# Optimization experiments

Hardware: AMD Instinct MI355X
Metric: run time of the kernel (lower is better)

Reference implementation:

```python
import jax, jax.numpy as jnp
import numpy as np

B, S, HID = 2, 2048, 2048
H, HK, D = 16, 4, 128  # num_heads, num_kv_heads, head_dim
G = H // HK            # GQA group size


def _make_rope(B, S, D):
    pos = jnp.arange(S, dtype=jnp.float32)
    inv_freq = 1.0 / (10000.0 ** (jnp.arange(0, D, 2, dtype=jnp.float32) / D))
    freqs = pos[:, None] * inv_freq[None, :]          # [S, D/2]
    emb = jnp.concatenate([freqs, freqs], axis=-1)     # [S, D]
    cos = jnp.broadcast_to(jnp.cos(emb)[None], (B, S, D))
    sin = jnp.broadcast_to(jnp.sin(emb)[None], (B, S, D))
    return cos, sin


def setup_inputs() -> dict:
    key = jax.random.key(0)
    k0, k1, k2 = jax.random.split(key, 3)
    hidden_states = jax.random.normal(k0, (B, S, HID), dtype=jnp.float32)
    cos, sin = _make_rope(B, S, D)
    w_qkv = jax.random.normal(k1, ((H + 2 * HK) * D, HID), dtype=jnp.float32) * 0.02
    b_qkv = jnp.zeros(((H + 2 * HK) * D,), dtype=jnp.float32)
    w_o = jax.random.normal(k2, (HID, HID), dtype=jnp.float32) * 0.02
    b_o = jnp.zeros((HID,), dtype=jnp.float32)
    return {"hidden_states": hidden_states, "cos": cos, "sin": sin,
            "w_qkv": w_qkv, "b_qkv": b_qkv, "w_o": w_o, "b_o": b_o}


def _rotate_half(x):
    x1, x2 = jnp.split(x, 2, axis=-1)
    return jnp.concatenate([-x2, x1], axis=-1)


def reference(hidden_states, cos, sin, w_qkv, b_qkv, w_o, b_o):
    b, s, _ = hidden_states.shape
    qkv = jnp.einsum('bsh,oh->bso', hidden_states, w_qkv) + b_qkv
    q, k, v = jnp.split(qkv, [H * D, (H + HK) * D], axis=-1)
    # [B, heads, S, D]
    q = q.reshape(b, s, H, D).transpose(0, 2, 1, 3)
    k = k.reshape(b, s, HK, D).transpose(0, 2, 1, 3)
    v = v.reshape(b, s, HK, D).transpose(0, 2, 1, 3)
    # RoPE (cos/sin broadcast over head axis)
    c = cos[:, None, :, :]
    sn = sin[:, None, :, :]
    q = q * c + _rotate_half(q) * sn
    k = k * c + _rotate_half(k) * sn
    # GQA attention without materializing repeated K/V: group q heads
    qg = q.reshape(b, HK, G, s, D)
    scale = 1.0 / jnp.sqrt(jnp.float32(D))
    scores = jnp.einsum('bkgqd,bkpd->bkgqp', qg, k) * scale  # [B,HK,G,S,S]
    probs = jax.nn.softmax(scores, axis=-1)
    out = jnp.einsum('bkgqp,bkpd->bkgqd', probs, v)           # [B,HK,G,S,D]
    out = out.reshape(b, H, s, D).transpose(0, 2, 1, 3).reshape(b, s, H * D)
    return jnp.einsum('bsh,oh->bso', out, w_o) + b_o
```

## Files before the change

kernel.cpp:

```cpp
#include <hip/hip_runtime.h>
#include <hip/hip_bf16.h>
#include <stdint.h>

typedef __bf16 bf16x8 __attribute__((ext_vector_type(8)));
typedef float f32x4 __attribute__((ext_vector_type(4)));
typedef float f32x16 __attribute__((ext_vector_type(16)));
typedef float f32x4v __attribute__((ext_vector_type(4)));
typedef unsigned short u16;
typedef unsigned int u32;
typedef u16 u16x8 __attribute__((ext_vector_type(8)));
typedef u32 u32x4 __attribute__((ext_vector_type(4)));

#define B_ 2
#define S_ 2048
#define HID_ 2048
#define H_ 16
#define HK_ 4
#define D_ 128
#define NQKV_ 3072

__device__ __forceinline__ u16 f2bf(float f) {
  u32 u = __builtin_bit_cast(u32, f);
  u32 r = (u + 0x7fffu + ((u >> 16) & 1u)) >> 16;
  return (u16)r;
}
__device__ __forceinline__ float bf2f(u16 v) {
  u32 u = ((u32)v) << 16;
  return __builtin_bit_cast(float, u);
}
__device__ __forceinline__ u32 cvtpk(float lo, float hi) {
  u32 r;
  asm("v_cvt_pk_bf16_f32 %0, %1, %2" : "=v"(r) : "v"(lo), "v"(hi));
  return r;
}
__device__ __forceinline__ void gload_lds16(const void* g, void* l) {
  __builtin_amdgcn_global_load_lds((const __attribute__((address_space(1))) void*)g,
                                   (__attribute__((address_space(3))) void*)l, 16, 0, 0);
}

__global__ __launch_bounds__(256) void k_cvt3(const float* __restrict__ a, u16* __restrict__ oa, int na,
                                              const float* __restrict__ b, u16* __restrict__ ob, int nb,
                                              const float* __restrict__ c, u16* __restrict__ oc, int nc) {
  int total = na + nb + nc;
  for (int i = blockIdx.x * 256 + threadIdx.x; i < total; i += gridDim.x * 256) {
    const float* src;
    u16* dst;
    int j = i;
    if (j < na) { src = a; dst = oa; }
    else if (j < na + nb) { j -= na; src = b; dst = ob; }
    else { j -= na + nb; src = c; dst = oc; }
    const f32x4v* p = (const f32x4v*)(src + (size_t)j * 8);
    f32x4v x = p[0], y = p[1];
    u16x8 w;
    w[0] = f2bf(x[0]); w[1] = f2bf(x[1]); w[2] = f2bf(x[2]); w[3] = f2bf(x[3]);
    w[4] = f2bf(y[0]); w[5] = f2bf(y[1]); w[6] = f2bf(y[2]); w[7] = f2bf(y[3]);
    *(u16x8*)(dst + (size_t)j * 8) = w;
  }
}

template <int ISSUES>
__device__ __forceinline__ void stage_half(const u16* __restrict__ src, int K, char* ldsb, int tid) {
#pragma unroll
  for (int i = 0; i < ISSUES; ++i) {
    int off = i * 8192 + tid * 16;
    int r = off >> 7, cb = off & 127;
    int scb = cb ^ ((r & 7) << 4);
    gload_lds16((const char*)(src + (size_t)r * K) + scb, ldsb + i * 8192 + (tid & ~63) * 16);
  }
}

template <int BM, typename CT>
__global__ __launch_bounds__(512, 1) void k_gemm8p(const u16* __restrict__ A, const u16* __restrict__ Bm,
                                                   const float* __restrict__ bias, CT* __restrict__ C,
                                                   int M, int N, int K) {
  constexpr int HAR = BM / 2;
  constexpr int AHB = HAR * 128;
  constexpr int AISS = AHB / 8192;
  constexpr int MREP = BM / 32;
  constexpr int MQ = MREP / 4;
  constexpr int DB = 2 * AHB + 32768;
  __shared__ __attribute__((aligned(16))) char lds[2 * DB];
  const int tid = threadIdx.x, lane = tid & 63;
  const int wid = tid >> 6, wm = wid >> 2, wn = wid & 3;
  const int l15 = lane & 15, l4 = lane >> 4;
  const int nwg = gridDim.x * gridDim.y;
  const int bid = blockIdx.y * gridDim.x + blockIdx.x;
  const int wgid = (bid & 7) * (nwg >> 3) + (bid >> 3);
  const int bx = wgid % gridDim.x, by = wgid / gridDim.x;
  const int row0 = by * BM, col0 = bx * 256;
  const int NT = K >> 6;

  f32x4 acc[MREP][4] = {};

  auto stageA = [&](int t, int h) {
    stage_half<AISS>(A + (size_t)(row0 + h * HAR) * K + t * 64, K, lds + (t & 1) * DB + h * AHB, tid);
  };
  auto stageB = [&](int t, int h) {
    stage_half<2>(Bm + (size_t)(col0 + h * 128) * K + t * 64, K, lds + (t & 1) * DB + 2 * AHB + h * 16384, tid);
  };

  stageA(0, 0); stageA(0, 1); stageB(0, 0); stageB(0, 1);
  if (NT > 1) { stageB(1, 0); stageB(1, 1); }
  if (NT > 1) asm volatile("s_waitcnt vmcnt(4)" ::: "memory");
  else        asm volatile("s_waitcnt vmcnt(0)" ::: "memory");
  __builtin_amdgcn_s_barrier();

  const char* myA = lds + wm * AHB;
  const char* myB = lds + 2 * AHB + (wn >> 1) * 16384;
  const int rBb = (wn & 1) * 64;

  for (int t = 0; t < NT; ++t) {
    const int d = t & 1;
    const char* Ab = myA + d * DB;
    const char* Bb = myB + d * DB;
    bf16x8 bfr[4][2];
#pragma unroll
    for (int j = 0; j < 4; ++j) {
      if (j == 0) {
#pragma unroll
        for (int n = 0; n < 4; ++n)
#pragma unroll
          for (int ks = 0; ks < 2; ++ks) {
            int r = rBb + n * 16 + l15;
            bfr[n][ks] = *(const bf16x8*)(Bb + r * 128 + ((ks * 64 + l4 * 16) ^ ((r & 7) << 4)));
          }
      }
      bf16x8 afr[MQ][2];
#pragma unroll
      for (int mq = 0; mq < MQ; ++mq)
#pragma unroll
        for (int ks = 0; ks < 2; ++ks) {
          int r = (j * MQ + mq) * 16 + l15;
          afr[mq][ks] = *(const bf16x8*)(Ab + r * 128 + ((ks * 64 + l4 * 16) ^ ((r & 7) << 4)));
        }
      if (j == 0) { if (t + 1 < NT) stageA(t + 1, 0); }
      else if (j == 1) { if (t + 1 < NT) stageA(t + 1, 1); }
      else if (j == 2) { if (t + 2 < NT) stageB(t + 2, 0); }
      else {
        if (t + 2 < NT) { stageB(t + 2, 1); asm volatile("s_waitcnt vmcnt(4)" ::: "memory"); }
        else             asm volatile("s_waitcnt vmcnt(0)" ::: "memory");
      }
      __builtin_amdgcn_s_barrier();
      asm volatile("s_waitcnt lgkmcnt(0)" ::: "memory");
      __builtin_amdgcn_s_setprio(1);
#pragma unroll
      for (int mq = 0; mq < MQ; ++mq)
#pragma unroll
        for (int ks = 0; ks < 2; ++ks)
#pragma unroll
          for (int n = 0; n < 4; ++n)
            acc[j * MQ + mq][n] =
                __builtin_amdgcn_mfma_f32_16x16x32_bf16(afr[mq][ks], bfr[n][ks], acc[j * MQ + mq][n], 0, 0, 0);
      __builtin_amdgcn_s_setprio(0);
      __builtin_amdgcn_s_barrier();
    }
  }

#pragma unroll
  for (int m = 0; m < MREP; ++m) {
    int grow = row0 + wm * HAR + m * 16 + l4 * 4;
#pragma unroll
    for (int n = 0; n < 4; ++n) {
      int gcol = col0 + wn * 64 + n * 16 + l15;
      float bv = bias[gcol];
#pragma unroll
      for (int r2 = 0; r2 < 4; ++r2) {
        float v = acc[m][n][r2] + bv;
        if constexpr (sizeof(CT) == 2) C[(size_t)(grow + r2) * N + gcol] = (CT)f2bf(v);
        else                           C[(size_t)(grow + r2) * N + gcol] = v;
      }
    }
  }
}

__global__ __launch_bounds__(256) void k_rope_split(const u16* __restrict__ qkv,
                                                    const float* __restrict__ cosb,
                                                    const float* __restrict__ sinb,
                                                    u16* __restrict__ Qb, u16* __restrict__ Kb,
                                                    u16* __restrict__ Vt) {
  const int bs = blockIdx.x;
  const int b = bs >> 11, s = bs & 2047;
  const size_t base = (size_t)bs * NQKV_;
  const size_t cs = (size_t)bs * D_;
  const int tid = threadIdx.x;
  const float qscale = 0.08838834764831845f;

  if (tid < 160) {
    const bool isq = tid < 128;
    const int idx = isq ? tid : (tid - 128);
    const int hh = idx >> 3, d0 = (idx & 7) * 8;
    const size_t srcb = base + (isq ? 0 : H_ * D_) + hh * D_;
    bf16x8 x1 = *(const bf16x8*)(qkv + srcb + d0);
    bf16x8 x2 = *(const bf16x8*)(qkv + srcb + d0 + 64);
    u16x8 y1, y2;
    const u16x8 u1 = __builtin_bit_cast(u16x8, x1);
    const u16x8 u2 = __builtin_bit_cast(u16x8, x2);
    const float sc = isq ? qscale : 1.0f;
#pragma unroll
    for (int i = 0; i < 8; ++i) {
      float f1 = bf2f(u1[i]), f2 = bf2f(u2[i]);
      float c1 = cosb[cs + d0 + i], s1 = sinb[cs + d0 + i];
      float c2 = cosb[cs + 64 + d0 + i], s2 = sinb[cs + 64 + d0 + i];
      y1[i] = f2bf((f1 * c1 - f2 * s1) * sc);
      y2[i] = f2bf((f2 * c2 + f1 * s2) * sc);
    }
    size_t o;
    if (isq) o = ((size_t)(b * H_ + hh) * S_ + s) * D_ + d0;
    else     o = ((size_t)(b * HK_ + hh) * S_ + s) * D_ + d0;
    u16* dst = isq ? Qb : Kb;
    *(u16x8*)(dst + o) = y1;
    *(u16x8*)(dst + o + 64) = y2;
  } else if (tid < 224) {
    const int idx = tid - 160;
    const int hk = idx >> 4, d0 = (idx & 15) * 8;
    bf16x8 xv = *(const bf16x8*)(qkv + base + (H_ + HK_) * D_ + hk * D_ + d0);
    const u16x8 uv = __builtin_bit_cast(u16x8, xv);
    u16* vb = Vt + (size_t)(b * HK_ + hk) * D_ * S_ + s;
#pragma unroll
    for (int i = 0; i < 8; ++i) vb[(size_t)(d0 + i) * S_] = uv[i];
  }
}

__global__ __launch_bounds__(512, 2) void k_attn(const u16* __restrict__ Qb, const u16* __restrict__ Kb,
                                                 const u16* __restrict__ Vt, u16* __restrict__ Ob) {
  __shared__ __attribute__((aligned(16))) char lds[65536];
  const int qt = blockIdx.x;
  const int bh = blockIdx.y;
  const int b = bh >> 4, h = bh & 15, hk = h >> 2;
  const int tid = threadIdx.x, lane = tid & 63, wid = tid >> 6;
  const int l31 = lane & 31, hi = lane >> 5;
  const int g = wid >> 2, wq = wid & 3;

  const int qrow = qt * 128 + wq * 32 + l31;
  const u16* qptr = Qb + ((size_t)(b * H_ + h) * S_ + qrow) * D_;
  bf16x8 qf[8];
#pragma unroll
  for (int ks = 0; ks < 8; ++ks) qf[ks] = *(const bf16x8*)(qptr + ks * 16 + hi * 8);

  const u16* kbase = Kb + (size_t)(b * HK_ + hk) * S_ * D_;
  const u16* vbase = Vt + (size_t)(b * HK_ + hk) * D_ * S_;
  char* gbase = lds + g * 32768;

  int krow[4], kc[4], vrow[4], vc[4];
#pragma unroll
  for (int i = 0; i < 4; ++i) {
    int s = (tid & 255) + i * 256;
    krow[i] = s >> 4; kc[i] = s & 15;
    vrow[i] = s >> 3; vc[i] = s & 7;
  }

  f32x16 o[4] = {};
  float mrun = -1e30f, lrun = 0.f;

  bf16x8 kreg[4], vreg[4];
  auto load_tile = [&](int tt) {
#pragma unroll
    for (int i = 0; i < 4; ++i) {
      kreg[i] = *(const bf16x8*)(kbase + (size_t)(tt * 64 + krow[i]) * D_ + kc[i] * 8);
      vreg[i] = *(const bf16x8*)(vbase + (size_t)vrow[i] * S_ + tt * 64 + vc[i] * 8);
    }
  };
  auto write_tile = [&]() {
#pragma unroll
    for (int i = 0; i < 4; ++i) {
      *(bf16x8*)(gbase + ((krow[i] * 256 + kc[i] * 16) ^ ((krow[i] & 15) << 4))) = kreg[i];
      *(bf16x8*)(gbase + 16384 + ((vrow[i] * 128 + vc[i] * 16) ^ ((vrow[i] & 7) << 4))) = vreg[i];
    }
  };

  const int t0 = g * 16;
  load_tile(t0);
  write_tile();
  __syncthreads();

  for (int t = 0; t < 16; ++t) {
    if (t < 15) load_tile(t0 + t + 1);

    f32x16 sc[2] = {};
    __builtin_amdgcn_s_setprio(1);
#pragma unroll
    for (int ks = 0; ks < 8; ++ks) {
#pragma unroll
      for (int T = 0; T < 2; ++T) {
        int row = T * 32 + l31;
        bf16x8 kf = *(const bf16x8*)(gbase + ((row * 256 + ks * 32 + hi * 16) ^ ((row & 15) << 4)));
        sc[T] = __builtin_amdgcn_mfma_f32_32x32x16_bf16(kf, qf[ks], sc[T], 0, 0, 0);
      }
    }
    __builtin_amdgcn_s_setprio(0);

    float pmax = sc[0][0];
#pragma unroll
    for (int r = 1; r < 16; ++r) pmax = fmaxf(pmax, sc[0][r]);
#pragma unroll
    for (int r = 0; r < 16; ++r) pmax = fmaxf(pmax, sc[1][r]);
    pmax = fmaxf(pmax, __shfl_xor(pmax, 32));
    if (__any(pmax > mrun + 8.f)) {
      float mn = fmaxf(mrun, pmax);
      float alpha = __expf(mrun - mn);
      mrun = mn;
      lrun *= alpha;
#pragma unroll
      for (int dt = 0; dt < 4; ++dt)
#pragma unroll
        for (int r = 0; r < 16; ++r) o[dt][r] *= alpha;
    }
    float rs = 0.f;
#pragma unroll
    for (int T = 0; T < 2; ++T)
#pragma unroll
      for (int r = 0; r < 16; ++r) {
        float p = __expf(sc[T][r] - mrun);
        sc[T][r] = p;
        rs += p;
      }
    rs += __shfl_xor(rs, 32);
    lrun += rs;

    bf16x8 pf[4];
#pragma unroll
    for (int T = 0; T < 2; ++T) {
#pragma unroll
      for (int gg = 0; gg < 2; ++gg) {
        u32 a0 = cvtpk(sc[T][8 * gg + 0], sc[T][8 * gg + 1]);
        u32 a1 = cvtpk(sc[T][8 * gg + 2], sc[T][8 * gg + 3]);
        u32 a2 = cvtpk(sc[T][8 * gg + 4], sc[T][8 * gg + 5]);
        u32 a3 = cvtpk(sc[T][8 * gg + 6], sc[T][8 * gg + 7]);
        u32 x0 = (u32)__shfl_xor((int)a0, 32);
        u32 x1 = (u32)__shfl_xor((int)a1, 32);
        u32 x2 = (u32)__shfl_xor((int)a2, 32);
        u32 x3 = (u32)__shfl_xor((int)a3, 32);
        u32 s0 = hi ? x2 : a0;
        u32 s1 = hi ? x3 : a1;
        u32 s2 = hi ? a2 : x0;
        u32 s3 = hi ? a3 : x1;
        u32x4 w = {s0, s1, s2, s3};
        pf[T * 2 + gg] = __builtin_bit_cast(bf16x8, w);
      }
    }

    __builtin_amdgcn_s_setprio(1);
#pragma unroll
    for (int ks2 = 0; ks2 < 4; ++ks2) {
#pragma unroll
      for (int dt = 0; dt < 4; ++dt) {
        int row = dt * 32 + l31;
        bf16x8 vf = *(const bf16x8*)(gbase + 16384 + ((row * 128 + ks2 * 32 + hi * 16) ^ ((row & 7) << 4)));
        o[dt] = __builtin_amdgcn_mfma_f32_32x32x16_bf16(vf, pf[ks2], o[dt], 0, 0, 0);
      }
    }
    __builtin_amdgcn_s_setprio(0);

    __syncthreads();
    if (t < 15) write_tile();
    __syncthreads();
  }

  float2* mlb = (float2*)(lds + 32768);
  if (g == 1) {
    char* myp = lds + wq * 8192;
#pragma unroll
    for (int dt = 0; dt < 4; ++dt)
#pragma unroll
      for (int t = 0; t < 8; ++t)
        *(u32*)(myp + (dt * 8 + t) * 256 + lane * 4) = cvtpk(o[dt][2 * t], o[dt][2 * t + 1]);
    if (!hi) mlb[wq * 32 + l31] = float2{mrun, lrun};
  }
  __syncthreads();
  float inv = 0.f;
  if (g == 0) {
    float2 ml1 = mlb[wq * 32 + l31];
    float m = fmaxf(mrun, ml1.x);
    float a0 = __expf(mrun - m), a1 = __expf(ml1.x - m);
    float lt = lrun * a0 + ml1.y * a1;
    inv = 1.0f / lt;
    char* myp = lds + wq * 8192;
#pragma unroll
    for (int dt = 0; dt < 4; ++dt)
#pragma unroll
      for (int t = 0; t < 8; ++t) {
        u32 w = *(const u32*)(myp + (dt * 8 + t) * 256 + lane * 4);
        float plo = bf2f((u16)(w & 0xffffu));
        float phi = bf2f((u16)(w >> 16));
        o[dt][2 * t]     = o[dt][2 * t] * a0 + plo * a1;
        o[dt][2 * t + 1] = o[dt][2 * t + 1] * a0 + phi * a1;
      }
  }
  __syncthreads();

  if (g == 0) {
    char* myreg = lds + wq * 8192;
#pragma unroll
    for (int dt = 0; dt < 4; ++dt)
#pragma unroll
      for (int t = 0; t < 8; ++t) {
        u32 w = cvtpk(o[dt][2 * t] * inv, o[dt][2 * t + 1] * inv);
        int d0 = dt * 32 + 2 * (t & 1) + 8 * (t >> 1) + 4 * hi;
        *(u32*)(myreg + ((l31 * 256 + d0 * 2) ^ ((l31 & 15) << 4))) = w;
      }
    asm volatile("s_waitcnt lgkmcnt(0)");
    {
      int q = lane >> 1, hf = lane & 1;
      int srow = qt * 128 + wq * 32 + q;
      u16* orow = Ob + ((size_t)(b * S_ + srow)) * HID_ + h * 128 + hf * 64;
#pragma unroll
      for (int i = 0; i < 8; ++i) {
        bf16x8 vv = *(const bf16x8*)(myreg + ((q * 256 + hf * 128 + i * 16) ^ ((q & 15) << 4)));
        *(bf16x8*)(orow + i * 8) = vv;
      }
    }
  }
}

extern "C" void kernel_launch(void* const* d_in, const int* in_sizes, int n_in,
                              void* d_out, int out_size, void* d_ws, size_t ws_size,
                              hipStream_t stream) {
  const float* hs = (const float*)d_in[0];
  const float* cosb = (const float*)d_in[1];
  const float* sinb = (const float*)d_in[2];
  const float* w_qkv = (const float*)d_in[3];
  const float* b_qkv = (const float*)d_in[4];
  const float* w_o = (const float*)d_in[5];
  const float* b_o = (const float*)d_in[6];
  float* out = (float*)d_out;

  char* ws = (char*)d_ws;
  u16* Xb    = (u16*)ws;
  u16* Wqkvb = (u16*)(ws + 16777216);
  u16* Wob   = (u16*)(ws + 29360128);
  u16* qkvb  = (u16*)(ws + 37748736);
  u16* Qb    = (u16*)(ws + 62914560);
  u16* Kb    = (u16*)(ws + 79691776);
  u16* Vt    = (u16*)(ws + 83886080);
  u16* Ob = Xb;

  hipLaunchKernelGGL(k_cvt3, dim3(2048), dim3(256), 0, stream,
                     hs, Xb, (B_ * S_ * HID_) / 8,
                     w_qkv, Wqkvb, (NQKV_ * HID_) / 8,
                     w_o, Wob, (HID_ * HID_) / 8);
  hipLaunchKernelGGL((k_gemm8p<256, u16>), dim3(NQKV_ / 256, (B_ * S_) / 256), dim3(512), 0, stream,
                     Xb, Wqkvb, b_qkv, qkvb, B_ * S_, NQKV_, HID_);
  hipLaunchKernelGGL(k_rope_split, dim3(B_ * S_), dim3(256), 0, stream, qkvb, cosb, sinb, Qb, Kb, Vt);
  hipLaunchKernelGGL(k_attn, dim3(S_ / 128, B_ * H_), dim3(512), 0, stream, Qb, Kb, Vt, Ob);
  hipLaunchKernelGGL((k_gemm8p<128, float>), dim3(HID_ / 256, (B_ * S_) / 128), dim3(512), 0, stream,
                     Ob, Wob, b_o, out, B_ * S_, HID_, HID_);
}
```

Before: 228.4 us.

## Double-buffer K/V in LDS and double query rows per attention block

Each attention block now has 1024 threads and handles 256 query rows instead of 128, so one K/V tile in LDS serves eight query waves per group and global K/V traffic per query drops. K/V tiles are double-buffered in a 128KB LDS allocation, which removes one of the two barriers per iteration. In exchange the grid is halved, only one block fits per CU, and launch bounds of (1024,4) may force a tight register budget that causes spills.

```diff
diff --git a/kernel.cpp b/kernel.cpp
--- a/kernel.cpp
+++ b/kernel.cpp
@@ -221,17 +221,18 @@
   }
 }
 
-__global__ __launch_bounds__(512, 2) void k_attn(const u16* __restrict__ Qb, const u16* __restrict__ Kb,
-                                                 const u16* __restrict__ Vt, u16* __restrict__ Ob) {
-  __shared__ __attribute__((aligned(16))) char lds[65536];
+__global__ __launch_bounds__(1024, 4) void k_attn(const u16* __restrict__ Qb, const u16* __restrict__ Kb,
+                                                  const u16* __restrict__ Vt, u16* __restrict__ Ob) {
+  __shared__ __attribute__((aligned(16))) char lds[131072];
   const int qt = blockIdx.x;
   const int bh = blockIdx.y;
   const int b = bh >> 4, h = bh & 15, hk = h >> 2;
   const int tid = threadIdx.x, lane = tid & 63, wid = tid >> 6;
   const int l31 = lane & 31, hi = lane >> 5;
-  const int g = wid >> 2, wq = wid & 3;
-
-  const int qrow = qt * 128 + wq * 32 + l31;
+  const int g = wid >> 3, wq = wid & 7;
+  const int tid_g = tid & 511;
+
+  const int qrow = qt * 256 + wq * 32 + l31;
   const u16* qptr = Qb + ((size_t)(b * H_ + h) * S_ + qrow) * D_;
   bf16x8 qf[8];
 #pragma unroll
@@ -239,12 +240,12 @@
 
   const u16* kbase = Kb + (size_t)(b * HK_ + hk) * S_ * D_;
   const u16* vbase = Vt + (size_t)(b * HK_ + hk) * D_ * S_;
-  char* gbase = lds + g * 32768;
-
-  int krow[4], kc[4], vrow[4], vc[4];
-#pragma unroll
-  for (int i = 0; i < 4; ++i) {
-    int s = (tid & 255) + i * 256;
+  char* gregion = lds + g * 65536;
+
+  int krow[2], kc[2], vrow[2], vc[2];
+#pragma unroll
+  for (int i = 0; i < 2; ++i) {
+    int s = tid_g + i * 512;
     krow[i] = s >> 4; kc[i] = s & 15;
     vrow[i] = s >> 3; vc[i] = s & 7;
   }
@@ -252,28 +253,34 @@
   f32x16 o[4] = {};
   float mrun = -1e30f, lrun = 0.f;
 
-  bf16x8 kreg[4], vreg[4];
-  auto load_tile = [&](int tt) {
-#pragma unroll
-    for (int i = 0; i < 4; ++i) {
-      kreg[i] = *(const bf16x8*)(kbase + (size_t)(tt * 64 + krow[i]) * D_ + kc[i] * 8);
-      vreg[i] = *(const bf16x8*)(vbase + (size_t)vrow[i] * S_ + tt * 64 + vc[i] * 8);
+  bf16x8 kreg[2], vreg[2];
+  auto load_tile = [&](int T) {
+#pragma unroll
+    for (int i = 0; i < 2; ++i) {
+      kreg[i] = *(const bf16x8*)(kbase + (size_t)(T * 64 + krow[i]) * D_ + kc[i] * 8);
+      vreg[i] = *(const bf16x8*)(vbase + (size_t)vrow[i] * S_ + T * 64 + vc[i] * 8);
     }
   };
-  auto write_tile = [&]() {
-#pragma unroll
-    for (int i = 0; i < 4; ++i) {
-      *(bf16x8*)(gbase + ((krow[i] * 256 + kc[i] * 16) ^ ((krow[i] & 15) << 4))) = kreg[i];
-      *(bf16x8*)(gbase + 16384 + ((vrow[i] * 128 + vc[i] * 16) ^ ((vrow[i] & 7) << 4))) = vreg[i];
+  auto write_tile = [&](int d) {
+    char* nK = gregion + d * 32768;
+    char* nV = nK + 16384;
+#pragma unroll
+    for (int i = 0; i < 2; ++i) {
+      *(bf16x8*)(nK + ((krow[i] * 256 + kc[i] * 16) ^ ((krow[i] & 15) << 4))) = kreg[i];
+      *(bf16x8*)(nV + ((vrow[i] * 128 + vc[i] * 16) ^ ((vrow[i] & 7) << 4))) = vreg[i];
     }
   };
 
   const int t0 = g * 16;
   load_tile(t0);
-  write_tile();
+  write_tile(0);
   __syncthreads();
 
   for (int t = 0; t < 16; ++t) {
+    const int cur = t & 1;
+    const char* lKc = gregion + cur * 32768;
+    const char* lVc = lKc + 16384;
+
     if (t < 15) load_tile(t0 + t + 1);
 
     f32x16 sc[2] = {};
@@ -283,7 +290,7 @@
 #pragma unroll
       for (int T = 0; T < 2; ++T) {
         int row = T * 32 + l31;
-        bf16x8 kf = *(const bf16x8*)(gbase + ((row * 256 + ks * 32 + hi * 16) ^ ((row & 15) << 4)));
+        bf16x8 kf = *(const bf16x8*)(lKc + ((row * 256 + ks * 32 + hi * 16) ^ ((row & 15) << 4)));
         sc[T] = __builtin_amdgcn_mfma_f32_32x32x16_bf16(kf, qf[ks], sc[T], 0, 0, 0);
       }
     }
@@ -345,20 +352,19 @@
 #pragma unroll
       for (int dt = 0; dt < 4; ++dt) {
         int row = dt * 32 + l31;
-        bf16x8 vf = *(const bf16x8*)(gbase + 16384 + ((row * 128 + ks2 * 32 + hi * 16) ^ ((row & 7) << 4)));
+        bf16x8 vf = *(const bf16x8*)(lVc + ((row * 128 + ks2 * 32 + hi * 16) ^ ((row & 7) << 4)));
         o[dt] = __builtin_amdgcn_mfma_f32_32x32x16_bf16(vf, pf[ks2], o[dt], 0, 0, 0);
       }
     }
     __builtin_amdgcn_s_setprio(0);
 
+    if (t < 15) write_tile(cur ^ 1);
     __syncthreads();
-    if (t < 15) write_tile();
-    __syncthreads();
-  }
-
-  float2* mlb = (float2*)(lds + 32768);
+  }
+
+  float2* mlb = (float2*)lds;
   if (g == 1) {
-    char* myp = lds + wq * 8192;
+    char* myp = lds + 65536 + wq * 8192;
 #pragma unroll
     for (int dt = 0; dt < 4; ++dt)
 #pragma unroll
@@ -374,7 +380,7 @@
     float a0 = __expf(mrun - m), a1 = __expf(ml1.x - m);
     float lt = lrun * a0 + ml1.y * a1;
     inv = 1.0f / lt;
-    char* myp = lds + wq * 8192;
+    const char* myp = lds + 65536 + wq * 8192;
 #pragma unroll
     for (int dt = 0; dt < 4; ++dt)
 #pragma unroll
@@ -401,7 +407,7 @@
     asm volatile("s_waitcnt lgkmcnt(0)");
     {
       int q = lane >> 1, hf = lane & 1;
-      int srow = qt * 128 + wq * 32 + q;
+      int srow = qt * 256 + wq * 32 + q;
       u16* orow = Ob + ((size_t)(b * S_ + srow)) * HID_ + h * 128 + hf * 64;
 #pragma unroll
       for (int i = 0; i < 8; ++i) {
@@ -441,7 +447,7 @@
   hipLaunchKernelGGL((k_gemm8p<256, u16>), dim3(NQKV_ / 256, (B_ * S_) / 256), dim3(512), 0, stream,
                      Xb, Wqkvb, b_qkv, qkvb, B_ * S_, NQKV_, HID_);
   hipLaunchKernelGGL(k_rope_split, dim3(B_ * S_), dim3(256), 0, stream, qkvb, cosb, sinb, Qb, Kb, Vt);
-  hipLaunchKernelGGL(k_attn, dim3(S_ / 128, B_ * H_), dim3(512), 0, stream, Qb, Kb, Vt, Ob);
+  hipLaunchKernelGGL(k_attn, dim3(S_ / 256, B_ * H_), dim3(1024), 0, stream, Qb, Kb, Vt, Ob);
   hipLaunchKernelGGL((k_gemm8p<128, float>), dim3(HID_ / 256, (B_ * S_) / 128), dim3(512), 0, stream,
                      Ob, Wob, b_o, out, B_ * S_, HID_, HID_);
 }
```

Measured after the change: 434.7 us. +90.3%, slower.
